# Kernel tuning notes

Hardware: AMD Instinct MI355X
Metric: run time of the kernel (lower is better)

## Reference

```python
import jax, jax.numpy as jnp
import numpy as np

S, E, H, D, F = 2048, 1280, 16, 80, 5120
EPS = 1e-6


def _ln(x, g, b):
    m = x.mean(-1, keepdims=True)
    v = x.var(-1, keepdims=True)
    return (x - m) * jax.lax.rsqrt(v + EPS) * g + b


def _rotate_half(x):
    x1, x2 = jnp.split(x, 2, axis=-1)
    return jnp.concatenate([-x2, x1], axis=-1)


def _quick_gelu(x):
    return x * jax.nn.sigmoid(1.702 * x)


def setup_inputs() -> dict:
    key = jax.random.key(0)
    ks = jax.random.split(key, 12)
    inp = {
        "hidden_states": jax.random.normal(ks[0], (S, E), jnp.float32),
        "attention_mask": jnp.ones((1, 1, S, S), jnp.bool_),
        "cos": jax.random.uniform(ks[1], (S, D), jnp.float32),
        "sin": jax.random.uniform(ks[2], (S, D), jnp.float32),
        "ln1_g": jnp.ones((E,), jnp.float32),
        "ln1_b": jnp.zeros((E,), jnp.float32),
        "ln2_g": jnp.ones((E,), jnp.float32),
        "ln2_b": jnp.zeros((E,), jnp.float32),
        "w_qkv": jax.random.normal(ks[3], (E, 3 * E), jnp.float32) * (E ** -0.5),
        "b_qkv": jax.random.normal(ks[4], (3 * E,), jnp.float32) * 0.02,
        "w_o": jax.random.normal(ks[5], (E, E), jnp.float32) * (E ** -0.5),
        "b_o": jax.random.normal(ks[6], (E,), jnp.float32) * 0.02,
        "w_fc1": jax.random.normal(ks[7], (E, F), jnp.float32) * (E ** -0.5),
        "b_fc1": jax.random.normal(ks[8], (F,), jnp.float32) * 0.02,
        "w_fc2": jax.random.normal(ks[9], (F, E), jnp.float32) * (F ** -0.5),
        "b_fc2": jax.random.normal(ks[10], (E,), jnp.float32) * 0.02,
    }
    return inp


def reference(hidden_states, attention_mask, cos, sin, ln1_g, ln1_b, ln2_g, ln2_b,
              w_qkv, b_qkv, w_o, b_o, w_fc1, b_fc1, w_fc2, b_fc2):
    x = hidden_states  # [S, E]
    h = _ln(x, ln1_g, ln1_b)
    qkv = h @ w_qkv + b_qkv  # [S, 3E]
    q, k, v = jnp.split(qkv, 3, axis=-1)
    q = q.reshape(S, H, D)
    k = k.reshape(S, H, D)
    v = v.reshape(S, H, D)
    # rotary in fp32, cos/sin broadcast over head axis: [S, 1, D]
    c = cos[:, None, :].astype(jnp.float32)
    s = sin[:, None, :].astype(jnp.float32)
    qf, kf = q.astype(jnp.float32), k.astype(jnp.float32)
    q = (qf * c + _rotate_half(qf) * s).astype(q.dtype)
    k = (kf * c + _rotate_half(kf) * s).astype(k.dtype)
    # attention scores [H, S, S]
    scores = jnp.einsum('shd,thd->hst', q, k) / np.float32(np.sqrt(D))
    scores = jnp.where(attention_mask[0], scores, jnp.finfo(scores.dtype).min)
    probs = jax.nn.softmax(scores.astype(jnp.float32), axis=-1).astype(q.dtype)
    attn = jnp.einsum('hst,thd->shd', probs, v).reshape(S, E)
    attn = attn @ w_o + b_o
    x = x + attn
    h2 = _ln(x, ln2_g, ln2_b)
    mlp = _quick_gelu(h2 @ w_fc1 + b_fc1) @ w_fc2 + b_fc2
    return x + mlp
```

## Files before the change

### kernel.cpp

```cpp
#include <hip/hip_runtime.h>
#include <stdint.h>
#include <math.h>

#define S_LEN 2048
#define EMB   1280
#define NHEAD 16
#define HDIM  80
#define FDIM  5120

typedef __bf16 bf16x8 __attribute__((ext_vector_type(8)));
typedef float  f32x4  __attribute__((ext_vector_type(4)));
typedef int    i32x4  __attribute__((ext_vector_type(4)));
typedef unsigned short u16x8 __attribute__((ext_vector_type(8)));
typedef unsigned short u16x4 __attribute__((ext_vector_type(4)));

__device__ __forceinline__ float b2f(unsigned short u) {
    union { float f; unsigned int i; } x; x.i = ((unsigned int)u) << 16; return x.f;
}
__device__ __forceinline__ unsigned short f2b(float f) {
    union { float f; unsigned int i; } x; x.f = f;
    unsigned int r = x.i + 0x7FFFu + ((x.i >> 16) & 1u);
    return (unsigned short)(r >> 16);
}

__device__ __forceinline__ float wave_rsum(float v) {
    #pragma unroll
    for (int o = 32; o; o >>= 1) v += __shfl_down(v, o);
    return v;
}

__device__ __forceinline__ void trans64(
    const float* __restrict__ in, unsigned short* __restrict__ out,
    int R, int C, int bx, int by, int tid)
{
    __shared__ unsigned short tile[64][65];
    int c0 = bx * 64, r0 = by * 64;
    int tx = tid & 63, ty = tid >> 6;
    #pragma unroll
    for (int j = 0; j < 16; ++j) {
        int row = ty + j * 4;
        tile[row][tx] = f2b(in[(size_t)(r0 + row) * C + c0 + tx]);
    }
    __syncthreads();
    #pragma unroll
    for (int j = 0; j < 16; ++j) {
        int row = ty + j * 4;
        out[(size_t)(c0 + row) * R + r0 + tx] = tile[tx][row];
    }
}

__global__ __launch_bounds__(256) void transpose4_kernel(
    const float* __restrict__ w_qkv, unsigned short* __restrict__ wT_qkv,
    const float* __restrict__ w_o,   unsigned short* __restrict__ wT_o,
    const float* __restrict__ w_fc1, unsigned short* __restrict__ wT_fc1,
    const float* __restrict__ w_fc2, unsigned short* __restrict__ wT_fc2)
{
    int id = blockIdx.x, tid = threadIdx.x;
    if (id < 1200) {
        trans64(w_qkv, wT_qkv, 1280, 3840, id % 60, id / 60, tid);
    } else if (id < 1600) {
        int t = id - 1200;
        trans64(w_o, wT_o, 1280, 1280, t % 20, t / 20, tid);
    } else if (id < 3200) {
        int t = id - 1600;
        trans64(w_fc1, wT_fc1, 1280, 5120, t % 80, t / 80, tid);
    } else {
        int t = id - 3200;
        trans64(w_fc2, wT_fc2, 5120, 1280, t % 20, t / 20, tid);
    }
}

__global__ __launch_bounds__(256) void ln_kernel(
    const float* __restrict__ x,
    const float* __restrict__ g,
    const float* __restrict__ b,
    unsigned short* __restrict__ out)
{
    int row = blockIdx.x, tid = threadIdx.x;
    int lane = tid & 63, wave = tid >> 6;
    const float* xr = x + (size_t)row * EMB;
    float v[5], s = 0.f, ss = 0.f;
    #pragma unroll
    for (int i = 0; i < 5; ++i) {
        float f = xr[tid + i * 256];
        v[i] = f; s += f; ss += f * f;
    }
    s = wave_rsum(s); ss = wave_rsum(ss);
    __shared__ float rs[4], rss[4];
    if (lane == 0) { rs[wave] = s; rss[wave] = ss; }
    __syncthreads();
    float st  = rs[0] + rs[1] + rs[2] + rs[3];
    float sst = rss[0] + rss[1] + rss[2] + rss[3];
    float mean = st * (1.0f / EMB);
    float var  = sst * (1.0f / EMB) - mean * mean;
    float inv  = rsqrtf(var + 1e-6f);
    unsigned short* orow = out + (size_t)row * EMB;
    #pragma unroll
    for (int i = 0; i < 5; ++i) {
        int c = tid + i * 256;
        orow[c] = f2b((v[i] - mean) * inv * g[c] + b[c]);
    }
}

template<int EPI, int OM, int SPLIT>
__global__ __launch_bounds__(256) void gemm_kernel(
    const unsigned short* __restrict__ A,
    const unsigned short* __restrict__ Bt,
    const float* __restrict__ bias,
    const float* __restrict__ res,
    void* __restrict__ Cv,
    int M, int N, int K)
{
    __shared__ __align__(16) unsigned short As[2][128 * 32];
    __shared__ __align__(16) unsigned short Bs[2][128 * 32];

    int tid = threadIdx.x;
    int lane = tid & 63, wave = tid >> 6;
    int m0 = blockIdx.x * 128, n0 = blockIdx.y * 128;
    int wm = (wave >> 1) * 64, wn = (wave & 1) * 64;
    int kc = K / SPLIT;
    int kbeg = blockIdx.z * kc;
    const int NITER = kc / 32;

    f32x4 acc[4][4];
    #pragma unroll
    for (int i = 0; i < 4; ++i)
        #pragma unroll
        for (int j = 0; j < 4; ++j)
            acc[i][j] = (f32x4){0.f, 0.f, 0.f, 0.f};

    const unsigned short* Ap0 = A  + (size_t)(m0 + (tid >> 2)) * K + (tid & 3) * 8 + kbeg;
    const unsigned short* Ap1 = Ap0 + (size_t)64 * K;
    const unsigned short* Bp0 = Bt + (size_t)(n0 + (tid >> 2)) * K + (tid & 3) * 8 + kbeg;
    const unsigned short* Bp1 = Bp0 + (size_t)64 * K;

    int arow = lane & 15, aq = (lane >> 4) * 8;
    int aoff[4], boff[4];
    #pragma unroll
    for (int i = 0; i < 4; ++i) {
        aoff[i] = (wm + i * 16 + arow) * 32 + aq;
        boff[i] = (wn + i * 16 + arow) * 32 + aq;
    }

    i32x4 rA0a, rA1a, rB0a, rB1a, rA0b, rA1b, rB0b, rB1b;

    rA0b = *(const i32x4*)(Ap0);
    rA1b = *(const i32x4*)(Ap1);
    rB0b = *(const i32x4*)(Bp0);
    rB1b = *(const i32x4*)(Bp1);
    *(i32x4*)&As[0][tid * 8]        = rA0b;
    *(i32x4*)&As[0][2048 + tid * 8] = rA1b;
    *(i32x4*)&Bs[0][tid * 8]        = rB0b;
    *(i32x4*)&Bs[0][2048 + tid * 8] = rB1b;
    if (NITER > 1) {
        rA0a = *(const i32x4*)(Ap0 + 32);
        rA1a = *(const i32x4*)(Ap1 + 32);
        rB0a = *(const i32x4*)(Bp0 + 32);
        rB1a = *(const i32x4*)(Bp1 + 32);
    }
    __syncthreads();

#define GSTEP(IT, AW0, AW1, BW0, BW1, AL0, AL1, BL0, BL1)                    \
    {                                                                         \
        const int cur = (IT) & 1, nb = cur ^ 1;                               \
        if ((IT) + 1 < NITER) {                                               \
            *(i32x4*)&As[nb][tid * 8]        = AW0;                           \
            *(i32x4*)&As[nb][2048 + tid * 8] = AW1;                           \
            *(i32x4*)&Bs[nb][tid * 8]        = BW0;                           \
            *(i32x4*)&Bs[nb][2048 + tid * 8] = BW1;                           \
        }                                                                     \
        if ((IT) + 2 < NITER) {                                               \
            int ko = ((IT) + 2) * 32;                                         \
            AL0 = *(const i32x4*)(Ap0 + ko);                                  \
            AL1 = *(const i32x4*)(Ap1 + ko);                                  \
            BL0 = *(const i32x4*)(Bp0 + ko);                                  \
            BL1 = *(const i32x4*)(Bp1 + ko);                                  \
        }                                                                     \
        bf16x8 af[4], bfm[4];                                                 \
        _Pragma("unroll") for (int i = 0; i < 4; ++i) {                       \
            af[i]  = *(const bf16x8*)&As[cur][aoff[i]];                       \
            bfm[i] = *(const bf16x8*)&Bs[cur][boff[i]];                       \
        }                                                                     \
        _Pragma("unroll") for (int mi = 0; mi < 4; ++mi)                      \
            _Pragma("unroll") for (int ni = 0; ni < 4; ++ni)                  \
                acc[mi][ni] = __builtin_amdgcn_mfma_f32_16x16x32_bf16(        \
                    af[mi], bfm[ni], acc[mi][ni], 0, 0, 0);                   \
        __syncthreads();                                                      \
    }

    for (int it = 0; it < NITER; it += 2) {
        GSTEP(it,     rA0a, rA1a, rB0a, rB1a, rA0b, rA1b, rB0b, rB1b)
        GSTEP(it + 1, rA0b, rA1b, rB0b, rB1b, rA0a, rA1a, rB0a, rB1a)
    }
#undef GSTEP

    int col = lane & 15;
    int rbase = (lane >> 4) * 4;
    #pragma unroll
    for (int ni = 0; ni < 4; ++ni) {
        int gn = n0 + wn + ni * 16 + col;
        float bv = (OM == 2) ? 0.f : bias[gn];
        #pragma unroll
        for (int mi = 0; mi < 4; ++mi) {
            int gm = m0 + wm + mi * 16 + rbase;
            #pragma unroll
            for (int r = 0; r < 4; ++r) {
                float v = acc[mi][ni][r] + bv;
                if (OM != 2) {
                    if (EPI == 1) v = v / (1.0f + expf(-1.702f * v));
                }
                if (OM == 2)
                    ((float*)Cv)[((size_t)blockIdx.z * M + gm + r) * N + gn] = v;
                else if (OM == 1)
                    ((float*)Cv)[(size_t)(gm + r) * N + gn] = v;
                else
                    ((unsigned short*)Cv)[(size_t)(gm + r) * N + gn] = f2b(v);
            }
        }
    }
}

template<int Z>
__global__ __launch_bounds__(256) void reduceZ_kernel(
    const float* __restrict__ part,
    const float* __restrict__ res,
    const float* __restrict__ bias,
    float* __restrict__ out)
{
    size_t i4 = ((size_t)blockIdx.x * 256 + threadIdx.x) * 4;
    int colb = (int)(i4 % EMB);
    f32x4 a = *(const f32x4*)&res[i4];
    f32x4 bv = *(const f32x4*)&bias[colb];
    a += bv;
    const size_t slice = (size_t)S_LEN * EMB;
    #pragma unroll
    for (int z = 0; z < Z; ++z)
        a += *(const f32x4*)&part[z * slice + i4];
    *(f32x4*)&out[i4] = a;
}

__global__ __launch_bounds__(256) void ropev_kernel(
    const unsigned short* __restrict__ qkv,
    const float* __restrict__ cosb,
    const float* __restrict__ sinb,
    unsigned short* __restrict__ q_out,
    unsigned short* __restrict__ k_out,
    unsigned short* __restrict__ vt)
{
    __shared__ unsigned short qT[64 * 84];
    __shared__ unsigned short kT[64 * 84];
    __shared__ unsigned short vT[64 * 84];

    int h = blockIdx.x >> 5, stile = blockIdx.x & 31;
    int s0 = stile * 64;
    int tid = threadIdx.x;

    u16x4 qr[5], kr[5];
    #pragma unroll
    for (int i = 0; i < 5; ++i) {
        int u = tid + i * 256;
        int row = u / 20, col = (u % 20) * 4;
        const unsigned short* base = qkv + (size_t)(s0 + row) * (3 * EMB) + h * HDIM + col;
        qr[i] = *(const u16x4*)base;
        kr[i] = *(const u16x4*)(base + EMB);
        u16x4 v4 = *(const u16x4*)(base + 2 * EMB);
        *(u16x4*)&qT[row * 84 + col] = qr[i];
        *(u16x4*)&kT[row * 84 + col] = kr[i];
        *(u16x4*)&vT[row * 84 + col] = v4;
    }
    __syncthreads();

    #pragma unroll
    for (int i = 0; i < 5; ++i) {
        int u = tid + i * 256;
        int row = u / 20, col = (u % 20) * 4;
        int pcol = (col < 40) ? col + 40 : col - 40;
        float sgn = (col < 40) ? -1.f : 1.f;
        u16x4 qp = *(const u16x4*)&qT[row * 84 + pcol];
        u16x4 kp = *(const u16x4*)&kT[row * 84 + pcol];
        f32x4 c4 = *(const f32x4*)&cosb[(size_t)(s0 + row) * HDIM + col];
        f32x4 s4 = *(const f32x4*)&sinb[(size_t)(s0 + row) * HDIM + col];
        u16x4 qo, ko;
        #pragma unroll
        for (int j = 0; j < 4; ++j) {
            qo[j] = f2b(b2f(qr[i][j]) * c4[j] + sgn * b2f(qp[j]) * s4[j]);
            ko[j] = f2b(b2f(kr[i][j]) * c4[j] + sgn * b2f(kp[j]) * s4[j]);
        }
        size_t o = ((size_t)h * S_LEN + s0 + row) * HDIM + col;
        *(u16x4*)&q_out[o] = qo;
        *(u16x4*)&k_out[o] = ko;
    }
    #pragma unroll
    for (int i = 0; i < 5; ++i) {
        int w = tid + i * 256;
        int d = w >> 4, c4i = (w & 15) * 4;
        u16x4 pk;
        #pragma unroll
        for (int j = 0; j < 4; ++j) pk[j] = vT[(c4i + j) * 84 + d];
        *(u16x4*)(vt + ((size_t)h * HDIM + d) * S_LEN + s0 + c4i) = pk;
    }
}

__global__ __launch_bounds__(256) void fattn_kernel(
    const unsigned short* __restrict__ q,
    const unsigned short* __restrict__ k,
    const unsigned short* __restrict__ vt,
    unsigned short* __restrict__ out)
{
    __shared__ __align__(16) unsigned short Qs[64 * 96];
    __shared__ __align__(16) unsigned short Ks[2][64 * 96];
    __shared__ __align__(16) unsigned short Vs[2][80 * 72];
    __shared__ __align__(16) unsigned short Pt[4 * 16 * 72];

    int tid = threadIdx.x;
    int lane = tid & 63, wave = tid >> 6;
    int arow = lane & 15, quad = lane >> 4;
    int h = blockIdx.x >> 5, qb = blockIdx.x & 31;
    int s0 = qb * 64;
    const float c = 0.16129856f;

    const unsigned short* qbase = q + ((size_t)h * S_LEN + s0) * HDIM;
    const unsigned short* kbase = k + (size_t)h * S_LEN * HDIM;
    const unsigned short* vbase = vt + (size_t)h * HDIM * S_LEN;

    #pragma unroll
    for (int i = 0; i < 5; ++i) {
        int u = tid + i * 256;
        int row = u / 20, col = (u % 20) * 4;
        u16x4 qv = *(const u16x4*)(qbase + u * 4);
        u16x4 qs4;
        #pragma unroll
        for (int j = 0; j < 4; ++j) qs4[j] = f2b(b2f(qv[j]) * c);
        *(u16x4*)&Qs[row * 96 + col] = qs4;
    }
    {
        int zr = tid >> 2, zc = 80 + (tid & 3) * 4;
        *(u16x4*)&Qs[zr * 96 + zc]    = (u16x4){0, 0, 0, 0};
        *(u16x4*)&Ks[0][zr * 96 + zc] = (u16x4){0, 0, 0, 0};
        *(u16x4*)&Ks[1][zr * 96 + zc] = (u16x4){0, 0, 0, 0};
    }

    u16x4 kreg[5], vreg[5];
    #pragma unroll
    for (int i = 0; i < 5; ++i) {
        int u = tid + i * 256;
        kreg[i] = *(const u16x4*)(kbase + u * 4);
        vreg[i] = *(const u16x4*)(vbase + (size_t)(u >> 4) * S_LEN + (u & 15) * 4);
    }
    #pragma unroll
    for (int i = 0; i < 5; ++i) {
        int u = tid + i * 256;
        *(u16x4*)&Ks[0][(u / 20) * 96 + (u % 20) * 4] = kreg[i];
        *(u16x4*)&Vs[0][(u >> 4) * 72 + (u & 15) * 4] = vreg[i];
    }
    #pragma unroll
    for (int i = 0; i < 5; ++i) {
        int u = tid + i * 256;
        kreg[i] = *(const u16x4*)(kbase + (size_t)64 * HDIM + u * 4);
        vreg[i] = *(const u16x4*)(vbase + (size_t)(u >> 4) * S_LEN + 64 + (u & 15) * 4);
    }
    __syncthreads();

    int pw = wave * 16 * 72;
    float l_part = 0.f;
    f32x4 o[5];
    #pragma unroll
    for (int di = 0; di < 5; ++di) o[di] = (f32x4){0.f, 0.f, 0.f, 0.f};

    const int NIT = S_LEN / 64;
    for (int it = 0; it < NIT; ++it) {
        int cur = it & 1;
        if (it + 1 < NIT) {
            int nb = (it + 1) & 1;
            #pragma unroll
            for (int i = 0; i < 5; ++i) {
                int u = tid + i * 256;
                *(u16x4*)&Ks[nb][(u / 20) * 96 + (u % 20) * 4] = kreg[i];
                *(u16x4*)&Vs[nb][(u >> 4) * 72 + (u & 15) * 4] = vreg[i];
            }
        }
        if (it + 2 < NIT) {
            int t0 = (it + 2) * 64;
            #pragma unroll
            for (int i = 0; i < 5; ++i) {
                int u = tid + i * 256;
                kreg[i] = *(const u16x4*)(kbase + (size_t)t0 * HDIM + u * 4);
                vreg[i] = *(const u16x4*)(vbase + (size_t)(u >> 4) * S_LEN + t0 + (u & 15) * 4);
            }
        }

        f32x4 sc[4];
        #pragma unroll
        for (int ni = 0; ni < 4; ++ni) sc[ni] = (f32x4){0.f, 0.f, 0.f, 0.f};
        #pragma unroll
        for (int kk = 0; kk < 3; ++kk) {
            bf16x8 bq = *(const bf16x8*)&Qs[(wave * 16 + arow) * 96 + kk * 32 + quad * 8];
            #pragma unroll
            for (int ni = 0; ni < 4; ++ni) {
                bf16x8 ak = *(const bf16x8*)&Ks[cur][(ni * 16 + arow) * 96 + kk * 32 + quad * 8];
                sc[ni] = __builtin_amdgcn_mfma_f32_16x16x32_bf16(ak, bq, sc[ni], 0, 0, 0);
            }
        }

        #pragma unroll
        for (int ni = 0; ni < 4; ++ni) {
            u16x4 pk;
            #pragma unroll
            for (int r = 0; r < 4; ++r) {
                float p = exp2f(sc[ni][r]);
                l_part += p;
                __bf16 pb = (__bf16)p;
                pk[r] = *(unsigned short*)&pb;
            }
            *(u16x4*)&Pt[pw + arow * 72 + ni * 16 + quad * 4] = pk;
        }

        #pragma unroll
        for (int kk = 0; kk < 2; ++kk) {
            bf16x8 ap = *(const bf16x8*)&Pt[pw + arow * 72 + kk * 32 + quad * 8];
            #pragma unroll
            for (int di = 0; di < 5; ++di) {
                bf16x8 bv = *(const bf16x8*)&Vs[cur][(di * 16 + arow) * 72 + kk * 32 + quad * 8];
                o[di] = __builtin_amdgcn_mfma_f32_16x16x32_bf16(ap, bv, o[di], 0, 0, 0);
            }
        }

        __syncthreads();
    }

    float l_run = l_part;
    l_run += __shfl_xor(l_run, 16);
    l_run += __shfl_xor(l_run, 32);

    float inv[4];
    #pragma unroll
    for (int r = 0; r < 4; ++r)
        inv[r] = 1.f / __shfl(l_run, (lane & 48) | (quad * 4 + r));
    #pragma unroll
    for (int r = 0; r < 4; ++r) {
        int gq = s0 + wave * 16 + quad * 4 + r;
        unsigned short* op = out + (size_t)gq * EMB + h * HDIM;
        #pragma unroll
        for (int di = 0; di < 5; ++di)
            op[di * 16 + arow] = f2b(o[di][r] * inv[r]);
    }
}

extern "C" void kernel_launch(void* const* d_in, const int* in_sizes, int n_in,
                              void* d_out, int out_size, void* d_ws, size_t ws_size,
                              hipStream_t stream)
{
    const float* hidden = (const float*)d_in[0];
    const float* cosb  = (const float*)d_in[2];
    const float* sinb  = (const float*)d_in[3];
    const float* ln1g  = (const float*)d_in[4];
    const float* ln1b  = (const float*)d_in[5];
    const float* ln2g  = (const float*)d_in[6];
    const float* ln2b  = (const float*)d_in[7];
    const float* w_qkv = (const float*)d_in[8];
    const float* b_qkv = (const float*)d_in[9];
    const float* w_o   = (const float*)d_in[10];
    const float* b_o   = (const float*)d_in[11];
    const float* w_fc1 = (const float*)d_in[12];
    const float* b_fc1 = (const float*)d_in[13];
    const float* w_fc2 = (const float*)d_in[14];
    const float* b_fc2 = (const float*)d_in[15];

    char* ws = (char*)d_ws;
    size_t off = 0;
    auto alloc = [&](size_t bytes) -> void* {
        void* p = (void*)(ws + off);
        off += (bytes + 255) & ~(size_t)255;
        return p;
    };
    unsigned short* wT_qkv = (unsigned short*)alloc((size_t)3840 * 1280 * 2);
    unsigned short* wT_o   = (unsigned short*)alloc((size_t)1280 * 1280 * 2);
    unsigned short* wT_fc1 = (unsigned short*)alloc((size_t)5120 * 1280 * 2);
    unsigned short* wT_fc2 = (unsigned short*)alloc((size_t)1280 * 5120 * 2);
    unsigned short* h1     = (unsigned short*)alloc((size_t)S_LEN * EMB * 2);
    unsigned short* qkv    = (unsigned short*)alloc((size_t)S_LEN * 3 * EMB * 2);
    unsigned short* q_r    = (unsigned short*)alloc((size_t)S_LEN * EMB * 2);
    unsigned short* k_r    = (unsigned short*)alloc((size_t)S_LEN * EMB * 2);
    unsigned short* vt_g   = (unsigned short*)alloc((size_t)S_LEN * EMB * 2);
    unsigned short* attn_o = (unsigned short*)alloc((size_t)S_LEN * EMB * 2);
    float*          x1     = (float*)alloc((size_t)S_LEN * EMB * 4);
    unsigned short* h2     = (unsigned short*)alloc((size_t)S_LEN * EMB * 2);
    unsigned short* mlp1   = (unsigned short*)alloc((size_t)S_LEN * FDIM * 2);
    float* partials = (float*)h1;

    transpose4_kernel<<<4800, 256, 0, stream>>>(
        w_qkv, wT_qkv, w_o, wT_o, w_fc1, wT_fc1, w_fc2, wT_fc2);

    ln_kernel<<<S_LEN, 256, 0, stream>>>(hidden, ln1g, ln1b, h1);

    gemm_kernel<0, 0, 1><<<dim3(S_LEN / 128, 3840 / 128, 1), 256, 0, stream>>>(
        h1, wT_qkv, b_qkv, nullptr, qkv, S_LEN, 3 * EMB, EMB);

    ropev_kernel<<<NHEAD * (S_LEN / 64), 256, 0, stream>>>(qkv, cosb, sinb, q_r, k_r, vt_g);

    fattn_kernel<<<NHEAD * (S_LEN / 64), 256, 0, stream>>>(q_r, k_r, vt_g, attn_o);

    gemm_kernel<0, 2, 2><<<dim3(S_LEN / 128, 1280 / 128, 2), 256, 0, stream>>>(
        attn_o, wT_o, b_o, nullptr, partials, S_LEN, EMB, EMB);
    reduceZ_kernel<2><<<(S_LEN * EMB / 4) / 256, 256, 0, stream>>>(
        partials, hidden, b_o, x1);

    ln_kernel<<<S_LEN, 256, 0, stream>>>(x1, ln2g, ln2b, h2);

    gemm_kernel<1, 0, 1><<<dim3(S_LEN / 128, FDIM / 128, 1), 256, 0, stream>>>(
        h2, wT_fc1, b_fc1, nullptr, mlp1, S_LEN, FDIM, EMB);

    gemm_kernel<0, 2, 4><<<dim3(S_LEN / 128, 1280 / 128, 4), 256, 0, stream>>>(
        mlp1, wT_fc2, b_fc2, nullptr, partials, S_LEN, EMB, FDIM);
    reduceZ_kernel<4><<<(S_LEN * EMB / 4) / 256, 256, 0, stream>>>(
        partials, x1, b_fc2, (float*)d_out);
}
```

Before: 371.7 us.

## Keep Q fragments in registers, swizzle K LDS layout, use hardware exp2 and setprio

The attention kernel now loads the scaled Q fragments straight into registers instead of staging them in shared memory. The K tile in LDS is stored with an XOR swizzle to reduce bank conflicts on the MFMA operand reads. exp2f is replaced with the raw hardware exp2 builtin, and s_setprio raises wave priority around the MFMA blocks. Holding Q in registers raises register pressure, and the fast exp2 may handle denormals or edge cases differently.

```diff
diff --git a/kernel.cpp b/kernel.cpp
--- a/kernel.cpp
+++ b/kernel.cpp
@@ -307,7 +307,6 @@
     const unsigned short* __restrict__ vt,
     unsigned short* __restrict__ out)
 {
-    __shared__ __align__(16) unsigned short Qs[64 * 96];
     __shared__ __align__(16) unsigned short Ks[2][64 * 96];
     __shared__ __align__(16) unsigned short Vs[2][80 * 72];
     __shared__ __align__(16) unsigned short Pt[4 * 16 * 72];
@@ -319,25 +318,30 @@
     int s0 = qb * 64;
     const float c = 0.16129856f;
 
-    const unsigned short* qbase = q + ((size_t)h * S_LEN + s0) * HDIM;
     const unsigned short* kbase = k + (size_t)h * S_LEN * HDIM;
     const unsigned short* vbase = vt + (size_t)h * HDIM * S_LEN;
 
-    #pragma unroll
-    for (int i = 0; i < 5; ++i) {
-        int u = tid + i * 256;
-        int row = u / 20, col = (u % 20) * 4;
-        u16x4 qv = *(const u16x4*)(qbase + u * 4);
-        u16x4 qs4;
-        #pragma unroll
-        for (int j = 0; j < 4; ++j) qs4[j] = f2b(b2f(qv[j]) * c);
-        *(u16x4*)&Qs[row * 96 + col] = qs4;
-    }
+    bf16x8 qf[3];
+    {
+        const unsigned short* qrp =
+            q + ((size_t)h * S_LEN + s0 + wave * 16 + arow) * HDIM;
+        #pragma unroll
+        for (int kk = 0; kk < 3; ++kk) {
+            int col = kk * 32 + quad * 8;
+            u16x8 qv = (u16x8){0, 0, 0, 0, 0, 0, 0, 0};
+            if (col < HDIM) qv = *(const u16x8*)(qrp + col);
+            u16x8 qs8;
+            #pragma unroll
+            for (int j = 0; j < 8; ++j) qs8[j] = f2b(b2f(qv[j]) * c);
+            qf[kk] = *(bf16x8*)&qs8;
+        }
+    }
+
     {
         int zr = tid >> 2, zc = 80 + (tid & 3) * 4;
-        *(u16x4*)&Qs[zr * 96 + zc]    = (u16x4){0, 0, 0, 0};
-        *(u16x4*)&Ks[0][zr * 96 + zc] = (u16x4){0, 0, 0, 0};
-        *(u16x4*)&Ks[1][zr * 96 + zc] = (u16x4){0, 0, 0, 0};
+        int zidx = (zr * 96 + zc) ^ ((zr & 7) << 3);
+        *(u16x4*)&Ks[0][zidx] = (u16x4){0, 0, 0, 0};
+        *(u16x4*)&Ks[1][zidx] = (u16x4){0, 0, 0, 0};
     }
 
     u16x4 kreg[5], vreg[5];
@@ -350,7 +354,8 @@
     #pragma unroll
     for (int i = 0; i < 5; ++i) {
         int u = tid + i * 256;
-        *(u16x4*)&Ks[0][(u / 20) * 96 + (u % 20) * 4] = kreg[i];
+        int row = u / 20, c4 = (u % 20) * 4;
+        *(u16x4*)&Ks[0][(row * 96 + c4) ^ ((row & 7) << 3)] = kreg[i];
         *(u16x4*)&Vs[0][(u >> 4) * 72 + (u & 15) * 4] = vreg[i];
     }
     #pragma unroll
@@ -360,6 +365,11 @@
         vreg[i] = *(const u16x4*)(vbase + (size_t)(u >> 4) * S_LEN + 64 + (u & 15) * 4);
     }
     __syncthreads();
+
+    int ksw[3];
+    #pragma unroll
+    for (int kk = 0; kk < 3; ++kk)
+        ksw[kk] = (arow * 96 + kk * 32 + quad * 8) ^ ((arow & 7) << 3);
 
     int pw = wave * 16 * 72;
     float l_part = 0.f;
@@ -375,7 +385,8 @@
             #pragma unroll
             for (int i = 0; i < 5; ++i) {
                 int u = tid + i * 256;
-                *(u16x4*)&Ks[nb][(u / 20) * 96 + (u % 20) * 4] = kreg[i];
+                int row = u / 20, c4 = (u % 20) * 4;
+                *(u16x4*)&Ks[nb][(row * 96 + c4) ^ ((row & 7) << 3)] = kreg[i];
                 *(u16x4*)&Vs[nb][(u >> 4) * 72 + (u & 15) * 4] = vreg[i];
             }
         }
@@ -392,22 +403,24 @@
         f32x4 sc[4];
         #pragma unroll
         for (int ni = 0; ni < 4; ++ni) sc[ni] = (f32x4){0.f, 0.f, 0.f, 0.f};
+        __builtin_amdgcn_s_setprio(1);
         #pragma unroll
         for (int kk = 0; kk < 3; ++kk) {
-            bf16x8 bq = *(const bf16x8*)&Qs[(wave * 16 + arow) * 96 + kk * 32 + quad * 8];
+            bf16x8 bq = qf[kk];
             #pragma unroll
             for (int ni = 0; ni < 4; ++ni) {
-                bf16x8 ak = *(const bf16x8*)&Ks[cur][(ni * 16 + arow) * 96 + kk * 32 + quad * 8];
+                bf16x8 ak = *(const bf16x8*)&Ks[cur][ksw[kk] + ni * 1536];
                 sc[ni] = __builtin_amdgcn_mfma_f32_16x16x32_bf16(ak, bq, sc[ni], 0, 0, 0);
             }
         }
+        __builtin_amdgcn_s_setprio(0);
 
         #pragma unroll
         for (int ni = 0; ni < 4; ++ni) {
             u16x4 pk;
             #pragma unroll
             for (int r = 0; r < 4; ++r) {
-                float p = exp2f(sc[ni][r]);
+                float p = __builtin_amdgcn_exp2f(sc[ni][r]);
                 l_part += p;
                 __bf16 pb = (__bf16)p;
                 pk[r] = *(unsigned short*)&pb;
@@ -415,6 +428,7 @@
             *(u16x4*)&Pt[pw + arow * 72 + ni * 16 + quad * 4] = pk;
         }
 
+        __builtin_amdgcn_s_setprio(1);
         #pragma unroll
         for (int kk = 0; kk < 2; ++kk) {
             bf16x8 ap = *(const bf16x8*)&Pt[pw + arow * 72 + kk * 32 + quad * 8];
@@ -424,6 +438,7 @@
                 o[di] = __builtin_amdgcn_mfma_f32_16x16x32_bf16(ap, bv, o[di], 0, 0, 0);
             }
         }
+        __builtin_amdgcn_s_setprio(0);
 
         __syncthreads();
     }
```

After: 362.7 us. 1.02x faster.
